# Optimization experiments

Hardware: AMD Instinct MI355X
Metric: run time of the kernel (lower is better)

Reference implementation:

```python
import jax, jax.numpy as jnp
import numpy as np

N_NODES = 50000
N_EDGES = 600000
N_RELS = 16
N_GRAPHS = 128
IN_DIM = 128
REL_LAYERS = [128, 256, 128]
HIDDEN = [128, 256, 128]
N_CLASSES = 8


def setup_inputs() -> dict:
    key = jax.random.key(0)
    ks = jax.random.split(key, 24)
    inp = {}
    inp["h"] = jax.random.normal(ks[0], (N_NODES, IN_DIM), dtype=jnp.float32)
    inp["src"] = jax.random.randint(ks[1], (N_EDGES,), 0, N_NODES)
    inp["dst"] = jax.random.randint(ks[2], (N_EDGES,), 0, N_NODES)
    inp["rel_types"] = jax.random.randint(ks[3], (N_EDGES,), 0, N_RELS)
    inp["graph_ids"] = jnp.sort(jax.random.randint(ks[4], (N_NODES,), 0, N_GRAPHS))
    # RelGraphConv params per layer: W_rel [R,din,dout], W_loop [din,dout], b [dout]
    prev = IN_DIM
    ki = 5
    for i, d in enumerate(REL_LAYERS):
        inp[f"W_rel{i}"] = jax.random.normal(ks[ki], (N_RELS, prev, d), dtype=jnp.float32) * 0.05
        inp[f"W_loop{i}"] = jax.random.normal(ks[ki + 1], (prev, d), dtype=jnp.float32) * 0.05
        inp[f"b{i}"] = jnp.zeros((d,), dtype=jnp.float32)
        prev = d
        ki += 2
    for i, d in enumerate(HIDDEN):
        inp[f"Wh{i}"] = jax.random.normal(ks[ki], (prev, d), dtype=jnp.float32) * 0.05
        inp[f"bh{i}"] = jnp.zeros((d,), dtype=jnp.float32)
        prev = d
        ki += 1
    inp["Wc"] = jax.random.normal(ks[ki], (prev, N_CLASSES), dtype=jnp.float32) * 0.05
    inp["bc"] = jnp.zeros((N_CLASSES,), dtype=jnp.float32)
    return inp


def _rel_graph_conv(h, src, dst, rel, W_rel, W_loop, b):
    # transform every node under every relation: [R, N, dout]
    t = jnp.einsum("nd,rde->rne", h, W_rel)
    msgs = t[rel, src]  # [E, dout] gather per edge
    agg = jax.ops.segment_sum(msgs, dst, num_segments=h.shape[0])
    return jax.nn.relu(agg + h @ W_loop + b)  # self-loop + bias (DGL defaults)


def _forward(h, src, dst, rel_types, graph_ids,
             W_rel0, W_loop0, b0, W_rel1, W_loop1, b1, W_rel2, W_loop2, b2,
             Wh0, bh0, Wh1, bh1, Wh2, bh2, Wc, bc):
    h = h.astype(jnp.float32)
    for Wr, Wl, b in ((W_rel0, W_loop0, b0), (W_rel1, W_loop1, b1), (W_rel2, W_loop2, b2)):
        h = _rel_graph_conv(h, src, dst, rel_types, Wr, Wl, b)
    # dgl.mean_nodes: per-graph mean pooling
    sums = jax.ops.segment_sum(h, graph_ids, num_segments=N_GRAPHS)
    cnts = jax.ops.segment_sum(jnp.ones((h.shape[0],), h.dtype), graph_ids, num_segments=N_GRAPHS)
    hg = sums / jnp.maximum(cnts, 1.0)[:, None]
    for W, b in ((Wh0, bh0), (Wh1, bh1), (Wh2, bh2)):
        hg = jax.nn.relu(hg @ W + b)
    return jax.nn.softmax(hg @ Wc + bc, axis=1)


def reference(h, src, dst, rel_types, graph_ids,
              W_rel0, W_loop0, b0, W_rel1, W_loop1, b1, W_rel2, W_loop2, b2,
              Wh0, bh0, Wh1, bh1, Wh2, bh2, Wc, bc):
    return _forward(h, src, dst, rel_types, graph_ids,
                    W_rel0, W_loop0, b0, W_rel1, W_loop1, b1, W_rel2, W_loop2, b2,
                    Wh0, bh0, Wh1, bh1, Wh2, bh2, Wc, bc)
```

## Files before the change

### kernel.cpp

```cpp
#include <hip/hip_runtime.h>
#include <stdint.h>

#define NN 50000
#define NE 600000
#define NR 16
#define NG 128
#define TS 128
#define SCAN_B 512
#define NB_SCAN ((NN + SCAN_B - 1) / SCAN_B)
#define MAXB 1024

typedef short bf16x8 __attribute__((ext_vector_type(8)));
typedef float f32x4 __attribute__((ext_vector_type(4)));

static __device__ __forceinline__ unsigned short f2bf(float x) {
    unsigned int b = __float_as_uint(x);
    b += 0x7FFFu + ((b >> 16) & 1u);
    return (unsigned short)(b >> 16);
}
static __device__ __forceinline__ float bf2f(unsigned short u) {
    return __uint_as_float(((unsigned int)u) << 16);
}


__global__ void k_hist(const int* __restrict__ rel, const int* __restrict__ dst,
                       const int* __restrict__ src,
                       int* __restrict__ bcnt, int* __restrict__ ncnt,
                       int npc, int nps, int SB, int B) {
    __shared__ int lh[MAXB];
    for (int i = threadIdx.x; i < B; i += 256) lh[i] = 0;
    __syncthreads();
    for (int e = blockIdx.x * blockDim.x + threadIdx.x; e < NE; e += gridDim.x * blockDim.x) {
        int d = dst[e];
        int key = (d / npc) * SB + (src[e] / nps) * NR + rel[e];
        atomicAdd(&lh[key], 1);
        atomicAdd(&ncnt[d], 1);
    }
    __syncthreads();
    for (int i = threadIdx.x; i < B; i += 256) atomicAdd(&bcnt[i], lh[i]);
}

__global__ void k_scan1(const int* __restrict__ ncnt, int* __restrict__ bsum) {
    __shared__ int s[SCAN_B];
    int i = blockIdx.x * SCAN_B + threadIdx.x;
    s[threadIdx.x] = (i < NN) ? ncnt[i] : 0;
    __syncthreads();
    for (int off = SCAN_B / 2; off > 0; off >>= 1) {
        if (threadIdx.x < off) s[threadIdx.x] += s[threadIdx.x + off];
        __syncthreads();
    }
    if (threadIdx.x == 0) bsum[blockIdx.x] = s[0];
}

__global__ void k_scan2(const int* __restrict__ bsum, int* __restrict__ bpref, int* __restrict__ rowptr) {
    if (threadIdx.x == 0 && blockIdx.x == 0) {
        int run = 0;
        for (int b = 0; b < NB_SCAN; ++b) { bpref[b] = run; run += bsum[b]; }
        rowptr[NN] = run;
    }
}

__global__ void k_scan3(const int* __restrict__ ncnt, const int* __restrict__ bpref,
                        int* __restrict__ rowptr) {
    __shared__ int s[SCAN_B];
    int i = blockIdx.x * SCAN_B + threadIdx.x;
    int val = (i < NN) ? ncnt[i] : 0;
    s[threadIdx.x] = val;
    __syncthreads();
    for (int off = 1; off < SCAN_B; off <<= 1) {
        int x = (threadIdx.x >= off) ? s[threadIdx.x - off] : 0;
        __syncthreads();
        s[threadIdx.x] += x;
        __syncthreads();
    }
    if (i < NN) rowptr[i] = bpref[blockIdx.x] + s[threadIdx.x] - val;
}

__global__ __launch_bounds__(1024)
void k_scan_buckets(const int* __restrict__ bcnt, int B, int npc, int SB,
                    const int* __restrict__ rowptr,
                    int* __restrict__ boff, int* __restrict__ tstart,
                    int4* __restrict__ tilemap) {
    __shared__ int s1[MAXB], s2[MAXB];
    __shared__ int e_ex[MAXB + 1], t_ex[MAXB + 1];
    int tid = threadIdx.x;
    int v1 = (tid < B) ? bcnt[tid] : 0;
    int v2 = (v1 + TS - 1) / TS;
    s1[tid] = v1; s2[tid] = v2;
    __syncthreads();
    for (int off = 1; off < MAXB; off <<= 1) {
        int a1 = (tid >= off) ? s1[tid - off] : 0;
        int a2 = (tid >= off) ? s2[tid - off] : 0;
        __syncthreads();
        s1[tid] += a1; s2[tid] += a2;
        __syncthreads();
    }
    if (tid < B) {
        e_ex[tid] = s1[tid] - v1;
        t_ex[tid] = s2[tid] - v2;
        boff[tid] = e_ex[tid];
        tstart[tid] = t_ex[tid];
        if (tid == B - 1) {
            e_ex[B] = s1[tid]; t_ex[B] = s2[tid];
            boff[B] = s1[tid]; tstart[B] = s2[tid];
        }
    }
    __syncthreads();
    int T = t_ex[B];
    for (int t = tid; t < T; t += 1024) {
        int lo = 0, hi = B - 1;
        while (lo < hi) {
            int mid = (lo + hi + 1) >> 1;
            if (t_ex[mid] <= t) lo = mid; else hi = mid - 1;
        }
        int b = lo;
        int tt = t - t_ex[b];
        int v1b = e_ex[b + 1] - e_ex[b];
        int rem = v1b - tt * TS;
        int cnt = rem < TS ? rem : TS;
        int chunk = b / SB;
        int nstart = chunk * npc; if (nstart > NN) nstart = NN;
        tilemap[t] = make_int4(b & (NR - 1), e_ex[b] + tt * TS, cnt, rowptr[nstart]);
    }
}

__global__ void k_scatter(const int* __restrict__ rel, const int* __restrict__ dst,
                          const int* __restrict__ src,
                          const int* __restrict__ boff, int* __restrict__ cursor,
                          const int* __restrict__ rowptr, int* __restrict__ ncur,
                          int* __restrict__ srcs, int* __restrict__ dpos,
                          int npc, int nps, int SB, int B) {
    __shared__ int lh[MAXB];
    const int CH = 4096;
    int e0 = blockIdx.x * CH;
    for (int i = threadIdx.x; i < B; i += 256) lh[i] = 0;
    __syncthreads();
    for (int i = threadIdx.x; i < CH; i += 256) {
        int e = e0 + i;
        if (e < NE) atomicAdd(&lh[(dst[e] / npc) * SB + (src[e] / nps) * NR + rel[e]], 1);
    }
    __syncthreads();
    for (int i = threadIdx.x; i < B; i += 256) {
        int c = lh[i];
        lh[i] = (c > 0) ? atomicAdd(&cursor[i], c) : 0;
    }
    __syncthreads();
    for (int i = threadIdx.x; i < CH; i += 256) {
        int e = e0 + i;
        if (e < NE) {
            int d = dst[e];
            int s = src[e];
            int b = (d / npc) * SB + (s / nps) * NR + rel[e];
            int p = boff[b] + atomicAdd(&lh[b], 1);
            int pd = rowptr[d] + atomicAdd(&ncur[d], 1);
            srcs[p] = s;
            dpos[p] = pd;
        }
    }
}


__global__ void k_hconv(const float* __restrict__ h, unsigned short* __restrict__ hb, int n4) {
    int i = blockIdx.x * 256 + threadIdx.x;
    if (i < n4) {
        float4 v = reinterpret_cast<const float4*>(h)[i];
        ushort4 o = { f2bf(v.x), f2bf(v.y), f2bf(v.z), f2bf(v.w) };
        reinterpret_cast<ushort4*>(hb)[i] = o;
    }
}

__global__ void k_wconv_all(const float* Wr0, const float* Wr1, const float* Wr2,
                            const float* Wl0, const float* Wl1, const float* Wl2,
                            unsigned short* Wt0, unsigned short* Wt1, unsigned short* Wt2,
                            unsigned short* Wlt0, unsigned short* Wlt1, unsigned short* Wlt2) {
    const float* W; unsigned short* O; int R, Kd, Nd;
    switch (blockIdx.y) {
        case 0:  W = Wr0; O = Wt0;  R = NR; Kd = 128; Nd = 128; break;
        case 1:  W = Wr1; O = Wt1;  R = NR; Kd = 128; Nd = 256; break;
        case 2:  W = Wr2; O = Wt2;  R = NR; Kd = 256; Nd = 128; break;
        case 3:  W = Wl0; O = Wlt0; R = 1;  Kd = 128; Nd = 128; break;
        case 4:  W = Wl1; O = Wlt1; R = 1;  Kd = 128; Nd = 256; break;
        default: W = Wl2; O = Wlt2; R = 1;  Kd = 256; Nd = 128; break;
    }
    int total = R * Kd * Nd;
    for (int i = blockIdx.x * 256 + threadIdx.x; i < total; i += gridDim.x * 256) {
        int r = i / (Kd * Nd);
        int rem = i - r * Kd * Nd;
        int k = rem / Nd;
        int n = rem - k * Nd;
        O[((size_t)r * Nd + n) * Kd + k] = f2bf(W[i]);
    }
}


template<int K>
__global__ __launch_bounds__(256, 4)
void k_dense_mfma(const unsigned short* __restrict__ hb,
                  const unsigned short* __restrict__ Wlt,
                  const float* __restrict__ bias,
                  float* __restrict__ outbuf, int ldn) {
    __shared__ __align__(16) unsigned short As[128][72];
    __shared__ __align__(16) unsigned short Bs[128][72];
    const int tid = threadIdx.x;
    const int row0 = blockIdx.x * 128;
    const int colbase = blockIdx.y * 128;
    const int lane = tid & 63, w = tid >> 6;
    const int quad = lane >> 4, col = lane & 15;
    const int srow = tid >> 3, sk = (tid & 7) * 8;

    f32x4 acc[8][2];
#pragma unroll
    for (int i = 0; i < 8; ++i) { acc[i][0] = 0.f; acc[i][1] = 0.f; }

    for (int k0 = 0; k0 < K; k0 += 64) {
        __syncthreads();
#pragma unroll
        for (int pp = 0; pp < 4; ++pp) {
            int rw = pp * 32 + srow;
            int ar = row0 + rw; if (ar >= NN) ar = NN - 1;
            *reinterpret_cast<uint4*>(&As[rw][sk]) =
                *reinterpret_cast<const uint4*>(hb + (size_t)ar * K + k0 + sk);
            *reinterpret_cast<uint4*>(&Bs[rw][sk]) =
                *reinterpret_cast<const uint4*>(Wlt + (size_t)(colbase + rw) * K + k0 + sk);
        }
        __syncthreads();
#pragma unroll
        for (int s = 0; s < 2; ++s) {
            bf16x8 bf0 = *reinterpret_cast<const bf16x8*>(&Bs[w * 32 + col][s * 32 + quad * 8]);
            bf16x8 bf1 = *reinterpret_cast<const bf16x8*>(&Bs[w * 32 + 16 + col][s * 32 + quad * 8]);
#pragma unroll
            for (int rt = 0; rt < 8; ++rt) {
                bf16x8 af = *reinterpret_cast<const bf16x8*>(&As[rt * 16 + col][s * 32 + quad * 8]);
                acc[rt][0] = __builtin_amdgcn_mfma_f32_16x16x32_bf16(af, bf0, acc[rt][0], 0, 0, 0);
                acc[rt][1] = __builtin_amdgcn_mfma_f32_16x16x32_bf16(af, bf1, acc[rt][1], 0, 0, 0);
            }
        }
    }
    float bv0 = bias[colbase + w * 32 + col];
    float bv1 = bias[colbase + w * 32 + 16 + col];
#pragma unroll
    for (int rt = 0; rt < 8; ++rt) {
#pragma unroll
        for (int reg = 0; reg < 4; ++reg) {
            int r = row0 + rt * 16 + quad * 4 + reg;
            if (r < NN) {
                float* dp = outbuf + (size_t)r * ldn + colbase + w * 32;
                dp[col] = acc[rt][0][reg] + bv0;
                dp[16 + col] = acc[rt][1][reg] + bv1;
            }
        }
    }
}


template<int K>
__global__ __launch_bounds__(256, 4)
void k_edge_mfma(const unsigned short* __restrict__ hb,
                 const unsigned short* __restrict__ Wt,
                 int ldn, int colbase, int msgw, int paired,
                 const int* __restrict__ srcs, const int* __restrict__ dpos,
                 const int4* __restrict__ tilemap, const int* __restrict__ tstart,
                 int chunkBase, int SB,
                 unsigned short* __restrict__ msg, int capRows) {
    const int tb0 = tstart[chunkBase];
    const int T = tstart[chunkBase + SB] - tb0;
    int t_lin, cb;
    if (paired) {
        t_lin = ((blockIdx.x >> 4) << 3) | (blockIdx.x & 7);
        cb = ((blockIdx.x >> 3) & 1) * 128;
    } else {
        t_lin = blockIdx.x;
        cb = colbase;
    }
    if (t_lin >= T) return;
    const int4 tm = tilemap[tb0 + t_lin];
    const int r = tm.x, e0 = tm.y, cnt = tm.z, cES = tm.w;

    __shared__ __align__(16) unsigned short As[128][136];
    __shared__ int s_src[TS], s_out[TS];
    const int tid = threadIdx.x;
    if (tid < TS) {
        int ei = e0 + (tid < cnt ? tid : cnt - 1);
        s_src[tid] = srcs[ei];
        int row = dpos[ei] - cES;
        s_out[tid] = (tid < cnt && row < capRows) ? row : -1;
    }
    __syncthreads();

    const unsigned short* Wb = Wt + ((size_t)r * ldn + cb) * K;
    const int lane = tid & 63, w = tid >> 6;
    const int quad = lane >> 4, col = lane & 15;
    const int asr = tid >> 4, ask = (tid & 15) * 8;

    f32x4 acc[8][2];
#pragma unroll
    for (int i = 0; i < 8; ++i) { acc[i][0] = 0.f; acc[i][1] = 0.f; }

    for (int kk = 0; kk < K; kk += 128) {
        if (kk) __syncthreads();
#pragma unroll
        for (int q = 0; q < 8; ++q) {
            int rw = q * 16 + asr;
            *reinterpret_cast<uint4*>(&As[rw][ask]) =
                *reinterpret_cast<const uint4*>(hb + (size_t)s_src[rw] * K + kk + ask);
        }
        __syncthreads();
#pragma unroll
        for (int k32 = 0; k32 < 4; ++k32) {
            bf16x8 bf0 = *reinterpret_cast<const bf16x8*>(
                Wb + (size_t)(w * 32 + col) * K + kk + k32 * 32 + quad * 8);
            bf16x8 bf1 = *reinterpret_cast<const bf16x8*>(
                Wb + (size_t)(w * 32 + 16 + col) * K + kk + k32 * 32 + quad * 8);
#pragma unroll
            for (int rt = 0; rt < 8; ++rt) {
                bf16x8 af = *reinterpret_cast<const bf16x8*>(&As[rt * 16 + col][k32 * 32 + quad * 8]);
                acc[rt][0] = __builtin_amdgcn_mfma_f32_16x16x32_bf16(af, bf0, acc[rt][0], 0, 0, 0);
                acc[rt][1] = __builtin_amdgcn_mfma_f32_16x16x32_bf16(af, bf1, acc[rt][1], 0, 0, 0);
            }
        }
    }
#pragma unroll
    for (int rt = 0; rt < 8; ++rt) {
#pragma unroll
        for (int reg = 0; reg < 4; ++reg) {
            int m = rt * 16 + quad * 4 + reg;
            int o = s_out[m];
            if (o >= 0) {
                unsigned short* dp = msg + (size_t)o * msgw + cb + w * 32;
                dp[col] = f2bf(acc[rt][0][reg]);
                dp[16 + col] = f2bf(acc[rt][1][reg]);
            }
        }
    }
}

__global__ __launch_bounds__(256)
void k_reduce(const unsigned short* __restrict__ msg, int msgw,
              const float* __restrict__ selfb, int ld_self, int co_self,
              unsigned short* __restrict__ out_bf, int ld_bf, int co_bf,
              float* __restrict__ out_f32, int ld_f32, int co_f32,
              const int* __restrict__ rowptr, int n0, int npc, int capRows) {
    int idx = blockIdx.x * 4 + (threadIdx.x >> 6);
    int n = n0 + idx;
    if (idx >= npc || n >= NN) return;
    int lane = threadIdx.x & 63;
    int cofs = blockIdx.y * 128;
    int cES = rowptr[n0];
    float2 acc = *reinterpret_cast<const float2*>(selfb + (size_t)n * ld_self + co_self + cofs + lane * 2);
    int j0 = rowptr[n], j1 = rowptr[n + 1];
    int jcap = cES + capRows; if (j1 > jcap) j1 = jcap;
    const int stride = msgw >> 1;
    const unsigned int* mp = reinterpret_cast<const unsigned int*>(msg) + (cofs >> 1) + lane;
    int j = j0;
    for (; j + 4 <= j1; j += 4) {
        unsigned int m0 = mp[(size_t)(j + 0 - cES) * stride];
        unsigned int m1 = mp[(size_t)(j + 1 - cES) * stride];
        unsigned int m2 = mp[(size_t)(j + 2 - cES) * stride];
        unsigned int m3 = mp[(size_t)(j + 3 - cES) * stride];
        acc.x += bf2f((unsigned short)(m0 & 0xffffu)) + bf2f((unsigned short)(m1 & 0xffffu))
               + bf2f((unsigned short)(m2 & 0xffffu)) + bf2f((unsigned short)(m3 & 0xffffu));
        acc.y += bf2f((unsigned short)(m0 >> 16)) + bf2f((unsigned short)(m1 >> 16))
               + bf2f((unsigned short)(m2 >> 16)) + bf2f((unsigned short)(m3 >> 16));
    }
    for (; j < j1; ++j) {
        unsigned int m = mp[(size_t)(j - cES) * stride];
        acc.x += bf2f((unsigned short)(m & 0xffffu));
        acc.y += bf2f((unsigned short)(m >> 16));
    }
    acc.x = acc.x > 0.f ? acc.x : 0.f;
    acc.y = acc.y > 0.f ? acc.y : 0.f;
    if (out_bf) {
        unsigned int o = (unsigned int)f2bf(acc.x) | ((unsigned int)f2bf(acc.y) << 16);
        *reinterpret_cast<unsigned int*>(out_bf + (size_t)n * ld_bf + co_bf + cofs + lane * 2) = o;
    }
    if (out_f32) {
        *reinterpret_cast<float2*>(out_f32 + (size_t)n * ld_f32 + co_f32 + cofs + lane * 2) = acc;
    }
}


__global__ void k_pool(const float* __restrict__ h, const int* __restrict__ gid,
                       float* __restrict__ hg, float* __restrict__ gcnt) {
    const int c = threadIdx.x;
    int n0 = blockIdx.x * 64;
    if (n0 >= NN) return;
    int end = n0 + 64; if (end > NN) end = NN;
    int cur = gid[n0];
    float run = 0.f, crun = 0.f;
    for (int n = n0; n < end; ++n) {
        int g = gid[n];
        if (g != cur) {
            atomicAdd(&hg[cur * 128 + c], run);
            if (c == 0) atomicAdd(&gcnt[cur], crun);
            run = 0.f; crun = 0.f; cur = g;
        }
        run += h[(size_t)n * 128 + c];
        crun += 1.f;
    }
    atomicAdd(&hg[cur * 128 + c], run);
    if (c == 0) atomicAdd(&gcnt[cur], crun);
}

__global__ __launch_bounds__(256)
void k_head(const float* __restrict__ hg, const float* __restrict__ gcnt,
            const float* __restrict__ Wh0, const float* __restrict__ bh0,
            const float* __restrict__ Wh1, const float* __restrict__ bh1,
            const float* __restrict__ Wh2, const float* __restrict__ bh2,
            const float* __restrict__ Wc, const float* __restrict__ bc,
            float* __restrict__ out) {
    __shared__ float x0[128], x1[128], x2[256], x3[128], sl[8];
    int g = blockIdx.x, t = threadIdx.x;
    if (t < 128) {
        float c = gcnt[g];
        x0[t] = hg[g * 128 + t] / (c > 1.f ? c : 1.f);
    }
    __syncthreads();
    if (t < 128) {
        float a = bh0[t];
        for (int k = 0; k < 128; ++k) a += x0[k] * Wh0[k * 128 + t];
        x1[t] = a > 0.f ? a : 0.f;
    }
    __syncthreads();
    {
        float a = bh1[t];
        for (int k = 0; k < 128; ++k) a += x1[k] * Wh1[k * 256 + t];
        x2[t] = a > 0.f ? a : 0.f;
    }
    __syncthreads();
    if (t < 128) {
        float a = bh2[t];
        for (int k = 0; k < 256; ++k) a += x2[k] * Wh2[k * 128 + t];
        x3[t] = a > 0.f ? a : 0.f;
    }
    __syncthreads();
    if (t < 8) {
        float a = bc[t];
        for (int k = 0; k < 128; ++k) a += x3[k] * Wc[k * 8 + t];
        sl[t] = a;
    }
    __syncthreads();
    if (t == 0) {
        float m = sl[0];
        for (int c = 1; c < 8; ++c) m = sl[c] > m ? sl[c] : m;
        float s = 0.f, e[8];
        for (int c = 0; c < 8; ++c) { e[c] = expf(sl[c] - m); s += e[c]; }
        for (int c = 0; c < 8; ++c) out[g * 8 + c] = e[c] / s;
    }
}


extern "C" void kernel_launch(void* const* d_in, const int* in_sizes, int n_in,
                              void* d_out, int out_size, void* d_ws, size_t ws_size,
                              hipStream_t stream) {
    const float* h0   = (const float*)d_in[0];
    const int* src    = (const int*)d_in[1];
    const int* dst    = (const int*)d_in[2];
    const int* rel    = (const int*)d_in[3];
    const int* gid    = (const int*)d_in[4];
    const float* Wr0  = (const float*)d_in[5];
    const float* Wl0  = (const float*)d_in[6];
    const float* b0   = (const float*)d_in[7];
    const float* Wr1  = (const float*)d_in[8];
    const float* Wl1  = (const float*)d_in[9];
    const float* b1   = (const float*)d_in[10];
    const float* Wr2  = (const float*)d_in[11];
    const float* Wl2  = (const float*)d_in[12];
    const float* b2   = (const float*)d_in[13];
    const float* Wh0  = (const float*)d_in[14];
    const float* bh0  = (const float*)d_in[15];
    const float* Wh1  = (const float*)d_in[16];
    const float* bh1  = (const float*)d_in[17];
    const float* Wh2  = (const float*)d_in[18];
    const float* bh2  = (const float*)d_in[19];
    const float* Wc   = (const float*)d_in[20];
    const float* bc   = (const float*)d_in[21];
    float* out = (float*)d_out;

    char* p = (char*)d_ws;
    auto alloc = [&](size_t bytes) { char* q = p; p += (bytes + 255) & ~(size_t)255; return q; };
    float* bufS  = (float*)alloc((size_t)NN * 256 * 4);
    unsigned short* hbA = (unsigned short*)alloc((size_t)NN * 256 * 2);
    unsigned short* hbB = (unsigned short*)alloc((size_t)NN * 128 * 2);
    unsigned short* Wt0 = (unsigned short*)alloc((size_t)NR * 128 * 128 * 2);
    unsigned short* Wt1 = (unsigned short*)alloc((size_t)NR * 256 * 128 * 2);
    unsigned short* Wt2 = (unsigned short*)alloc((size_t)NR * 128 * 256 * 2);
    unsigned short* Wlt0 = (unsigned short*)alloc((size_t)128 * 128 * 2);
    unsigned short* Wlt1 = (unsigned short*)alloc((size_t)256 * 128 * 2);
    unsigned short* Wlt2 = (unsigned short*)alloc((size_t)128 * 256 * 2);
    int* srcs    = (int*)alloc((size_t)NE * 4);
    int* dpos    = (int*)alloc((size_t)NE * 4);
    int* rowptr  = (int*)alloc((size_t)(NN + 1) * 4);
    int* bsum    = (int*)alloc(NB_SCAN * 4);
    int* bpref   = (int*)alloc(NB_SCAN * 4);
    int* boff    = (int*)alloc((MAXB + 1) * 4);
    int* tstart  = (int*)alloc((MAXB + 1) * 4);
    int4* tilemap = (int4*)alloc((size_t)(NE / TS + MAXB + 64) * 16);
    char* zbase  = p;
    int* bcnt    = (int*)alloc(MAXB * 4);
    int* cursor  = (int*)alloc(MAXB * 4);
    int* ncnt    = (int*)alloc((size_t)NN * 4);
    int* ncur    = (int*)alloc((size_t)NN * 4);
    float* hg    = (float*)alloc((size_t)NG * 128 * 4);
    float* gcnt  = (float*)alloc(NG * 4);
    size_t zlen  = (size_t)(p - zbase);
    unsigned short* msg = (unsigned short*)p;

    long long avail = (long long)ws_size - (long long)(p - (char*)d_ws);
    if (avail < (1 << 20)) avail = (1 << 20);
    long long capR64 = avail / 256;
    int C = 64;
    for (int c = 1; c <= 64; ++c) {
        double need = (double)NE / c * 1.15 + 4096.0;
        if ((double)capR64 >= need) { C = c; break; }
    }
    int npc = (NN + C - 1) / C;
    int S = MAXB / (C * NR); if (S < 1) S = 1;
    int SB = S * NR;
    int B = C * SB;
    int nps = (NN + S - 1) / S;
    int capRows = capR64 > 2000000000LL ? 2000000000 : (int)capR64;
    int TPC = (int)((double)NE / C * 1.15 / TS) + SB + 16;
    int RDB = (npc + 3) / 4;
    int fused = (C == 1 && (double)avail >= (double)NE * 1.15 * 512.0 + 2097152.0) ? 1 : 0;
    int capRows256 = (int)(avail / 512);

    hipMemsetAsync(zbase, 0, zlen, stream);
    k_hist<<<256, 256, 0, stream>>>(rel, dst, src, bcnt, ncnt, npc, nps, SB, B);
    k_scan1<<<NB_SCAN, SCAN_B, 0, stream>>>(ncnt, bsum);
    k_scan2<<<1, 64, 0, stream>>>(bsum, bpref, rowptr);
    k_scan3<<<NB_SCAN, SCAN_B, 0, stream>>>(ncnt, bpref, rowptr);
    k_scan_buckets<<<1, MAXB, 0, stream>>>(bcnt, B, npc, SB, rowptr, boff, tstart, tilemap);
    k_scatter<<<(NE + 4095) / 4096, 256, 0, stream>>>(rel, dst, src, boff, cursor, rowptr, ncur, srcs, dpos, npc, nps, SB, B);

    k_hconv<<<(NN * 128 / 4 + 255) / 256, 256, 0, stream>>>(h0, hbA, NN * 128 / 4);
    k_wconv_all<<<dim3(512, 6), 256, 0, stream>>>(Wr0, Wr1, Wr2, Wl0, Wl1, Wl2,
                                                  Wt0, Wt1, Wt2, Wlt0, Wlt1, Wlt2);

    const int RB = (NN + TS - 1) / TS;

    k_dense_mfma<128><<<dim3(RB, 1), 256, 0, stream>>>(hbA, Wlt0, b0, bufS, 128);
    for (int c = 0; c < C; ++c) {
        k_edge_mfma<128><<<TPC, 256, 0, stream>>>(hbA, Wt0, 128, 0, 128, 0, srcs, dpos, tilemap, tstart, c * SB, SB, msg, capRows);
        k_reduce<<<dim3(RDB, 1), 256, 0, stream>>>(msg, 128, bufS, 128, 0, hbB, 128, 0, (float*)nullptr, 0, 0, rowptr, c * npc, npc, capRows);
    }

    k_dense_mfma<128><<<dim3(RB, 2), 256, 0, stream>>>(hbB, Wlt1, b1, bufS, 256);
    if (fused) {
        k_edge_mfma<128><<<2 * TPC, 256, 0, stream>>>(hbB, Wt1, 256, 0, 256, 1, srcs, dpos, tilemap, tstart, 0, SB, msg, capRows256);
        k_reduce<<<dim3(RDB, 2), 256, 0, stream>>>(msg, 256, bufS, 256, 0, hbA, 256, 0, (float*)nullptr, 0, 0, rowptr, 0, npc, capRows256);
    } else {
        for (int half = 0; half < 2; ++half) {
            for (int c = 0; c < C; ++c) {
                k_edge_mfma<128><<<TPC, 256, 0, stream>>>(hbB, Wt1, 256, half * 128, 128, 0, srcs, dpos, tilemap, tstart, c * SB, SB, msg, capRows);
                k_reduce<<<dim3(RDB, 1), 256, 0, stream>>>(msg, 128, bufS, 256, half * 128, hbA, 256, half * 128, (float*)nullptr, 0, 0, rowptr, c * npc, npc, capRows);
            }
        }
    }

    k_dense_mfma<256><<<dim3(RB, 1), 256, 0, stream>>>(hbA, Wlt2, b2, bufS, 128);
    for (int c = 0; c < C; ++c) {
        k_edge_mfma<256><<<TPC, 256, 0, stream>>>(hbA, Wt2, 128, 0, 128, 0, srcs, dpos, tilemap, tstart, c * SB, SB, msg, capRows);
        k_reduce<<<dim3(RDB, 1), 256, 0, stream>>>(msg, 128, bufS, 128, 0, (unsigned short*)nullptr, 0, 0, bufS, 128, 0, rowptr, c * npc, npc, capRows);
    }

    k_pool<<<(NN + 63) / 64, 128, 0, stream>>>(bufS, gid, hg, gcnt);
    k_head<<<NG, 256, 0, stream>>>(hg, gcnt, Wh0, bh0, Wh1, bh1, Wh2, bh2, Wc, bc, out);
}
```

Measured before the change: 751.8 us.

## Reorder CSR preprocessing so scatter computes per-dst counts and fixes offsets afterward

```diff
diff --git a/kernel.cpp b/kernel.cpp
--- a/kernel.cpp
+++ b/kernel.cpp
@@ -25,19 +25,75 @@
 
 __global__ void k_hist(const int* __restrict__ rel, const int* __restrict__ dst,
                        const int* __restrict__ src,
-                       int* __restrict__ bcnt, int* __restrict__ ncnt,
+                       int* __restrict__ bcnt,
                        int npc, int nps, int SB, int B) {
     __shared__ int lh[MAXB];
     for (int i = threadIdx.x; i < B; i += 256) lh[i] = 0;
     __syncthreads();
     for (int e = blockIdx.x * blockDim.x + threadIdx.x; e < NE; e += gridDim.x * blockDim.x) {
-        int d = dst[e];
-        int key = (d / npc) * SB + (src[e] / nps) * NR + rel[e];
+        int key = (dst[e] / npc) * SB + (src[e] / nps) * NR + rel[e];
         atomicAdd(&lh[key], 1);
-        atomicAdd(&ncnt[d], 1);
     }
     __syncthreads();
     for (int i = threadIdx.x; i < B; i += 256) atomicAdd(&bcnt[i], lh[i]);
+}
+
+__global__ __launch_bounds__(1024)
+void k_scanb(const int* __restrict__ bcnt, int B,
+             int* __restrict__ boff, int* __restrict__ tstart) {
+    __shared__ int s1[MAXB], s2[MAXB];
+    int tid = threadIdx.x;
+    int v1 = (tid < B) ? bcnt[tid] : 0;
+    int v2 = (v1 + TS - 1) / TS;
+    s1[tid] = v1; s2[tid] = v2;
+    __syncthreads();
+    for (int off = 1; off < MAXB; off <<= 1) {
+        int a1 = (tid >= off) ? s1[tid - off] : 0;
+        int a2 = (tid >= off) ? s2[tid - off] : 0;
+        __syncthreads();
+        s1[tid] += a1; s2[tid] += a2;
+        __syncthreads();
+    }
+    if (tid < B) {
+        boff[tid] = s1[tid] - v1;
+        tstart[tid] = s2[tid] - v2;
+        if (tid == B - 1) { boff[B] = s1[tid]; tstart[B] = s2[tid]; }
+    }
+}
+
+__global__ void k_scatter(const int* __restrict__ rel, const int* __restrict__ dst,
+                          const int* __restrict__ src,
+                          const int* __restrict__ boff, int* __restrict__ cursor,
+                          int* __restrict__ ncur,
+                          int* __restrict__ srcs, int* __restrict__ dstv, int* __restrict__ dpos,
+                          int npc, int nps, int SB, int B) {
+    __shared__ int lh[MAXB];
+    const int CH = 4096;
+    int e0 = blockIdx.x * CH;
+    for (int i = threadIdx.x; i < B; i += 256) lh[i] = 0;
+    __syncthreads();
+    for (int i = threadIdx.x; i < CH; i += 256) {
+        int e = e0 + i;
+        if (e < NE) atomicAdd(&lh[(dst[e] / npc) * SB + (src[e] / nps) * NR + rel[e]], 1);
+    }
+    __syncthreads();
+    for (int i = threadIdx.x; i < B; i += 256) {
+        int c = lh[i];
+        lh[i] = (c > 0) ? atomicAdd(&cursor[i], c) : 0;
+    }
+    __syncthreads();
+    for (int i = threadIdx.x; i < CH; i += 256) {
+        int e = e0 + i;
+        if (e < NE) {
+            int d = dst[e];
+            int s = src[e];
+            int b = (d / npc) * SB + (s / nps) * NR + rel[e];
+            int p = boff[b] + atomicAdd(&lh[b], 1);
+            srcs[p] = s;
+            dstv[p] = d;
+            dpos[p] = atomicAdd(&ncur[d], 1);
+        }
+    }
 }
 
 __global__ void k_scan1(const int* __restrict__ ncnt, int* __restrict__ bsum) {
@@ -76,35 +132,19 @@
     if (i < NN) rowptr[i] = bpref[blockIdx.x] + s[threadIdx.x] - val;
 }
 
+__global__ void k_fix(const int* __restrict__ dstv, const int* __restrict__ rowptr,
+                      int* __restrict__ dpos) {
+    int p = blockIdx.x * 256 + threadIdx.x;
+    if (p < NE) dpos[p] += rowptr[dstv[p]];
+}
+
 __global__ __launch_bounds__(1024)
-void k_scan_buckets(const int* __restrict__ bcnt, int B, int npc, int SB,
-                    const int* __restrict__ rowptr,
-                    int* __restrict__ boff, int* __restrict__ tstart,
-                    int4* __restrict__ tilemap) {
-    __shared__ int s1[MAXB], s2[MAXB];
+void k_tilemap(const int* __restrict__ boff, const int* __restrict__ tstart,
+               int B, int npc, int SB,
+               const int* __restrict__ rowptr, int4* __restrict__ tilemap) {
     __shared__ int e_ex[MAXB + 1], t_ex[MAXB + 1];
     int tid = threadIdx.x;
-    int v1 = (tid < B) ? bcnt[tid] : 0;
-    int v2 = (v1 + TS - 1) / TS;
-    s1[tid] = v1; s2[tid] = v2;
-    __syncthreads();
-    for (int off = 1; off < MAXB; off <<= 1) {
-        int a1 = (tid >= off) ? s1[tid - off] : 0;
-        int a2 = (tid >= off) ? s2[tid - off] : 0;
-        __syncthreads();
-        s1[tid] += a1; s2[tid] += a2;
-        __syncthreads();
-    }
-    if (tid < B) {
-        e_ex[tid] = s1[tid] - v1;
-        t_ex[tid] = s2[tid] - v2;
-        boff[tid] = e_ex[tid];
-        tstart[tid] = t_ex[tid];
-        if (tid == B - 1) {
-            e_ex[B] = s1[tid]; t_ex[B] = s2[tid];
-            boff[B] = s1[tid]; tstart[B] = s2[tid];
-        }
-    }
+    for (int i = tid; i <= B; i += 1024) { e_ex[i] = boff[i]; t_ex[i] = tstart[i]; }
     __syncthreads();
     int T = t_ex[B];
     for (int t = tid; t < T; t += 1024) {
@@ -121,41 +161,6 @@
         int chunk = b / SB;
         int nstart = chunk * npc; if (nstart > NN) nstart = NN;
         tilemap[t] = make_int4(b & (NR - 1), e_ex[b] + tt * TS, cnt, rowptr[nstart]);
-    }
-}
-
-__global__ void k_scatter(const int* __restrict__ rel, const int* __restrict__ dst,
-                          const int* __restrict__ src,
-                          const int* __restrict__ boff, int* __restrict__ cursor,
-                          const int* __restrict__ rowptr, int* __restrict__ ncur,
-                          int* __restrict__ srcs, int* __restrict__ dpos,
-                          int npc, int nps, int SB, int B) {
-    __shared__ int lh[MAXB];
-    const int CH = 4096;
-    int e0 = blockIdx.x * CH;
-    for (int i = threadIdx.x; i < B; i += 256) lh[i] = 0;
-    __syncthreads();
-    for (int i = threadIdx.x; i < CH; i += 256) {
-        int e = e0 + i;
-        if (e < NE) atomicAdd(&lh[(dst[e] / npc) * SB + (src[e] / nps) * NR + rel[e]], 1);
-    }
-    __syncthreads();
-    for (int i = threadIdx.x; i < B; i += 256) {
-        int c = lh[i];
-        lh[i] = (c > 0) ? atomicAdd(&cursor[i], c) : 0;
-    }
-    __syncthreads();
-    for (int i = threadIdx.x; i < CH; i += 256) {
-        int e = e0 + i;
-        if (e < NE) {
-            int d = dst[e];
-            int s = src[e];
-            int b = (d / npc) * SB + (s / nps) * NR + rel[e];
-            int p = boff[b] + atomicAdd(&lh[b], 1);
-            int pd = rowptr[d] + atomicAdd(&ncur[d], 1);
-            srcs[p] = s;
-            dpos[p] = pd;
-        }
     }
 }
 
@@ -488,6 +493,7 @@
     unsigned short* Wlt1 = (unsigned short*)alloc((size_t)256 * 128 * 2);
     unsigned short* Wlt2 = (unsigned short*)alloc((size_t)128 * 256 * 2);
     int* srcs    = (int*)alloc((size_t)NE * 4);
+    int* dstv    = (int*)alloc((size_t)NE * 4);
     int* dpos    = (int*)alloc((size_t)NE * 4);
     int* rowptr  = (int*)alloc((size_t)(NN + 1) * 4);
     int* bsum    = (int*)alloc(NB_SCAN * 4);
@@ -498,7 +504,6 @@
     char* zbase  = p;
     int* bcnt    = (int*)alloc(MAXB * 4);
     int* cursor  = (int*)alloc(MAXB * 4);
-    int* ncnt    = (int*)alloc((size_t)NN * 4);
     int* ncur    = (int*)alloc((size_t)NN * 4);
     float* hg    = (float*)alloc((size_t)NG * 128 * 4);
     float* gcnt  = (float*)alloc(NG * 4);
@@ -525,12 +530,14 @@
     int capRows256 = (int)(avail / 512);
 
     hipMemsetAsync(zbase, 0, zlen, stream);
-    k_hist<<<256, 256, 0, stream>>>(rel, dst, src, bcnt, ncnt, npc, nps, SB, B);
-    k_scan1<<<NB_SCAN, SCAN_B, 0, stream>>>(ncnt, bsum);
+    k_hist<<<256, 256, 0, stream>>>(rel, dst, src, bcnt, npc, nps, SB, B);
+    k_scanb<<<1, MAXB, 0, stream>>>(bcnt, B, boff, tstart);
+    k_scatter<<<(NE + 4095) / 4096, 256, 0, stream>>>(rel, dst, src, boff, cursor, ncur, srcs, dstv, dpos, npc, nps, SB, B);
+    k_scan1<<<NB_SCAN, SCAN_B, 0, stream>>>(ncur, bsum);
     k_scan2<<<1, 64, 0, stream>>>(bsum, bpref, rowptr);
-    k_scan3<<<NB_SCAN, SCAN_B, 0, stream>>>(ncnt, bpref, rowptr);
-    k_scan_buckets<<<1, MAXB, 0, stream>>>(bcnt, B, npc, SB, rowptr, boff, tstart, tilemap);
-    k_scatter<<<(NE + 4095) / 4096, 256, 0, stream>>>(rel, dst, src, boff, cursor, rowptr, ncur, srcs, dpos, npc, nps, SB, B);
+    k_scan3<<<NB_SCAN, SCAN_B, 0, stream>>>(ncur, bpref, rowptr);
+    k_fix<<<(NE + 255) / 256, 256, 0, stream>>>(dstv, rowptr, dpos);
+    k_tilemap<<<1, MAXB, 0, stream>>>(boff, tstart, B, npc, SB, rowptr, tilemap);
 
     k_hconv<<<(NN * 128 / 4 + 255) / 256, 256, 0, stream>>>(h0, hbA, NN * 128 / 4);
     k_wconv_all<<<dim3(512, 6), 256, 0, stream>>>(Wr0, Wr1, Wr2, Wl0, Wl1, Wl2,
```

Measured after the change: 737.5 us. Within noise of the previous version (-1.9%).
